# Performance work log

Hardware: AMD Instinct MI355X
Metric: run time of the kernel (lower is better)

Reference implementation:

```python
import jax, jax.numpy as jnp
import numpy as np

LOCAL_RADIUS = 127          # block_len = 128
TOKENS_PER_BLOCK = 16       # global_seq_len = L // 16
NEG = -1e9


def _concat_3_blocks(x):
    # x: [B, nb, bl, H, d] -> [B, nb, 3*bl, H, d] (prev, cur, next block; zero-padded ends)
    p = jnp.pad(x, [(0, 0), (1, 1), (0, 0), (0, 0), (0, 0)])
    return jnp.concatenate([p[:, :-2], p[:, 1:-1], p[:, 2:]], axis=2)


def _softmax_with_extra_logit(x, axis=-1):
    m = jnp.maximum(jax.lax.stop_gradient(x.max(axis, keepdims=True)), 0)
    unnorm = jnp.exp(x - m)
    denom = unnorm.sum(axis, keepdims=True) + jnp.exp(-m)
    return unnorm / denom


def setup_inputs() -> dict:
    key = jax.random.key(0)
    ks = jax.random.split(key, 5)
    B, L, D, H, dh = 2, 4096, 1024, 16, 64
    return {
        "x": jax.random.normal(ks[0], (B, L, D), jnp.float32),
        "Wq": jax.random.normal(ks[1], (D, H, dh), jnp.float32) * 0.02,
        "Wk": jax.random.normal(ks[2], (D, H, dh), jnp.float32) * 0.02,
        "Wv": jax.random.normal(ks[3], (D, H, dh), jnp.float32) * 0.02,
        "Wo": jax.random.normal(ks[4], (H, dh, D), jnp.float32) * 0.02,
    }


def reference(x, Wq, Wk, Wv, Wo):
    B, L, D = x.shape
    H, dh = Wq.shape[1], Wq.shape[2]
    bl = LOCAL_RADIUS + 1                      # block_len = 128
    nb = L // bl                               # num_blocks
    G = L // TOKENS_PER_BLOCK                  # global (side) seq len

    q = jnp.einsum("bld,dhk->blhk", x, Wq) / jnp.sqrt(jnp.asarray(dh, x.dtype))
    k = jnp.einsum("bld,dhk->blhk", x, Wk)
    v = jnp.einsum("bld,dhk->blhk", x, Wv)

    # transient-global aggregates: sum token embeddings within each block of TOKENS_PER_BLOCK
    block_ids = jnp.arange(L) // TOKENS_PER_BLOCK          # [L]
    one_hot = jax.nn.one_hot(block_ids, G, dtype=x.dtype)  # [L, G]
    g = jnp.einsum("bld,lg->bgd", x, one_hot)              # [B, G, D]
    side_k = jnp.einsum("bgd,dhk->bghk", g, Wk)
    side_v = jnp.einsum("bgd,dhk->bghk", g, Wv)

    # split into blocks and build 3-block sliding window keys/values
    qb = q.reshape(B, nb, bl, H, dh)
    kb = _concat_3_blocks(k.reshape(B, nb, bl, H, dh))     # [B, nb, 3bl, H, dh]
    vb = _concat_3_blocks(v.reshape(B, nb, bl, H, dh))

    k_cat = jnp.concatenate(
        [kb, jnp.broadcast_to(side_k[:, None], (B, nb, G, H, dh))], axis=2)
    v_cat = jnp.concatenate(
        [vb, jnp.broadcast_to(side_v[:, None], (B, nb, G, H, dh))], axis=2)

    # logits: [B, nb, H, bl, 3bl+G]
    logits = jnp.einsum("bnqhd,bnkhd->bnhqk", qb, k_cat)

    # local mask: enforce |rel| <= local_radius and in-bounds key positions
    q_idx = jnp.arange(bl)[:, None]                        # [bl, 1]
    k_idx = jnp.arange(3 * bl)[None, :]                    # [1, 3bl]
    rel = k_idx - bl - q_idx                               # relative position
    b_idx = jnp.arange(nb)[:, None, None]                  # [nb, 1, 1]
    k_pos = (b_idx - 1) * bl + k_idx                       # absolute key position
    valid = (jnp.abs(rel) <= LOCAL_RADIUS) & (k_pos >= 0) & (k_pos < L)
    local_bias = jnp.where(valid, 0.0, NEG).astype(logits.dtype)  # [nb, bl, 3bl]
    side_bias = jnp.zeros((nb, bl, G), logits.dtype)
    bias = jnp.concatenate([local_bias, side_bias], axis=-1)      # [nb, bl, 3bl+G]
    logits = logits + bias[None, :, None]

    probs = _softmax_with_extra_logit(logits, axis=-1)
    y = jnp.einsum("bnhqk,bnkhd->bnqhd", probs, v_cat)
    y = y.reshape(B, L, H, dh)
    return jnp.einsum("blhk,hkd->bld", y, Wo)
```

## Files before the change

kernel.cpp:

```cpp
#include <hip/hip_runtime.h>
#include <hip/hip_bf16.h>
#include <stdint.h>

#define SC_LOG2E 0.18033688011112042f

typedef __attribute__((ext_vector_type(8))) short short8;
typedef __attribute__((ext_vector_type(4))) short short4v;
typedef __attribute__((ext_vector_type(4))) float f32x4;

__device__ __forceinline__ unsigned short f2bf(float f) {
  unsigned int u = __float_as_uint(f);
  u += 0x7fffu + ((u >> 16) & 1u);
  return (unsigned short)(u >> 16);
}

__device__ __forceinline__ unsigned int pkbf(float a, float b) {
  union { __hip_bfloat162 h; unsigned int u; } cv;
  cv.h = __float22bfloat162_rn(float2{a, b});
  return cv.u;
}

__device__ __forceinline__ void gload_lds16(const void* g, void* l) {
  __builtin_amdgcn_global_load_lds((const __attribute__((address_space(1))) void*)g,
                                   (__attribute__((address_space(3))) void*)l,
                                   16, 0, 0);
}

__device__ __forceinline__ f32x4 mfma16(short8 a, short8 b, f32x4 c) {
  return __builtin_amdgcn_mfma_f32_16x16x32_bf16(a, b, c, 0, 0, 0);
}

__device__ __forceinline__ short4v tr_read(const unsigned short* p) {
  short4v r;
  asm volatile("ds_read_b64_tr_b16 %0, %1"
               : "=v"(r)
               : "v"((const __attribute__((address_space(3))) unsigned short*)p));
  return r;
}

__device__ __forceinline__ short8 cat44(short4v lo, short4v hi) {
  return __builtin_shufflevector(lo, hi, 0, 1, 2, 3, 4, 5, 6, 7);
}

__global__ __launch_bounds__(256) void prep_k(
    const float* __restrict__ x, unsigned short* __restrict__ xb,
    const float* __restrict__ wq, const float* __restrict__ wk,
    const float* __restrict__ wv, const float* __restrict__ wo,
    unsigned short* __restrict__ wqkv_t, unsigned short* __restrict__ wo_t) {
  __shared__ float tile[64 * 65];
  int bid = blockIdx.x;
  if (bid < 512) {
    int gr = bid;
    int c4 = threadIdx.x;
    const float4* p = (const float4*)(x + (size_t)gr * 16384) + c4;
#pragma unroll
    for (int t = 0; t < 16; ++t) {
      float4 v = p[(size_t)t * 256];
      ushort4 o;
      o.x = f2bf(v.x); o.y = f2bf(v.y); o.z = f2bf(v.z); o.w = f2bf(v.w);
      ((ushort4*)xb)[(size_t)(gr * 16 + t) * 256 + c4] = o;
    }
  } else {
    int idx = bid - 512;
    int z = idx >> 8, rem = idx & 255;
    const float* src = (z == 0) ? wq : (z == 1) ? wk : (z == 2) ? wv : wo;
    unsigned short* dst = (z == 3) ? wo_t : (wqkv_t + (size_t)z * 1048576);
    float scale = (z == 0) ? SC_LOG2E : 1.0f;
    int tc = (rem & 15) * 64, tr = (rem >> 4) * 64;
    int cx = threadIdx.x & 63, ry = threadIdx.x >> 6;
#pragma unroll
    for (int i = 0; i < 16; ++i) {
      int r = ry + i * 4;
      tile[r * 65 + cx] = src[(size_t)(tr + r) * 1024 + tc + cx];
    }
    __syncthreads();
#pragma unroll
    for (int i = 0; i < 16; ++i) {
      int r = ry + i * 4;
      dst[(size_t)(tc + r) * 1024 + tr + cx] = f2bf(tile[cx * 65 + r] * scale);
    }
  }
}

template <bool F32OUT, bool SIDE>
__global__ __launch_bounds__(256) void gemm_bt_k(
    const unsigned short* __restrict__ A, const unsigned short* __restrict__ Bt,
    void* __restrict__ Cv, int M, int N, int K, int nbn,
    unsigned short* __restrict__ sidekv) {
  __shared__ unsigned short Alds[128 * 64];
  __shared__ unsigned short Blds[128 * 64];
  int bid = blockIdx.x;
  int bm = bid / nbn, bn = bid % nbn;
  int lane = threadIdx.x & 63, wid = threadIdx.x >> 6;
  int wr = wid >> 1, wc = wid & 1;
  int l15 = lane & 15, lg = lane >> 4;

  f32x4 zero4 = {0.f, 0.f, 0.f, 0.f};
  f32x4 acc[4][4];
#pragma unroll
  for (int i = 0; i < 4; ++i)
#pragma unroll
    for (int j = 0; j < 4; ++j) acc[i][j] = zero4;

  int srow[4], scol[4];
#pragma unroll
  for (int i = 0; i < 4; ++i) {
    int seg = wid * 4 + i;
    int r = seg * 8 + (lane >> 3);
    srow[i] = r;
    scol[i] = ((lane & 7) ^ (r & 7)) * 8;
  }
  size_t arow0 = (size_t)bm * 128, brow0 = (size_t)bn * 128;

  int ksteps = K >> 6;
  for (int ks = 0; ks < ksteps; ++ks) {
    int k0 = ks << 6;
#pragma unroll
    for (int i = 0; i < 4; ++i) {
      gload_lds16(A + (arow0 + srow[i]) * K + k0 + scol[i],
                  (char*)Alds + (wid * 4 + i) * 1024);
      gload_lds16(Bt + (brow0 + srow[i]) * K + k0 + scol[i],
                  (char*)Blds + (wid * 4 + i) * 1024);
    }
    __syncthreads();
#pragma unroll
    for (int kk = 0; kk < 2; ++kk) {
      short8 af[4], bfr[4];
#pragma unroll
      for (int mi = 0; mi < 4; ++mi) {
        int r = wr * 64 + mi * 16 + l15;
        af[mi] = *(const short8*)((const char*)Alds + r * 128 +
                                  ((kk * 64 + lg * 16) ^ ((r & 7) << 4)));
      }
#pragma unroll
      for (int ni = 0; ni < 4; ++ni) {
        int r = wc * 64 + ni * 16 + l15;
        bfr[ni] = *(const short8*)((const char*)Blds + r * 128 +
                                   ((kk * 64 + lg * 16) ^ ((r & 7) << 4)));
      }
#pragma unroll
      for (int mi = 0; mi < 4; ++mi)
#pragma unroll
        for (int ni = 0; ni < 4; ++ni)
          acc[mi][ni] = mfma16(af[mi], bfr[ni], acc[mi][ni]);
    }
    __syncthreads();
  }
  int rq = lg << 2;
#pragma unroll
  for (int mi = 0; mi < 4; ++mi) {
    size_t row = arow0 + wr * 64 + mi * 16 + rq;
#pragma unroll
    for (int ni = 0; ni < 4; ++ni) {
      size_t col = brow0 + wc * 64 + ni * 16 + l15;
#pragma unroll
      for (int r = 0; r < 4; ++r) {
        if (F32OUT)
          ((float*)Cv)[(row + r) * N + col] = acc[mi][ni][r];
        else
          ((unsigned short*)Cv)[(row + r) * N + col] = f2bf(acc[mi][ni][r]);
      }
    }
  }
  if (SIDE && bn >= 8) {
    int gg = bm * 8 + wr * 4;
    int colb = bn * 128 - 1024 + wc * 64;
#pragma unroll
    for (int mi = 0; mi < 4; ++mi) {
#pragma unroll
      for (int ni = 0; ni < 4; ++ni) {
        float s = (acc[mi][ni][0] + acc[mi][ni][1]) +
                  (acc[mi][ni][2] + acc[mi][ni][3]);
        s += __shfl_xor(s, 16);
        s += __shfl_xor(s, 32);
        if (lg == 0)
          sidekv[(size_t)(gg + mi) * 2048 + colb + ni * 16 + l15] = f2bf(s);
      }
    }
  }
}

__global__ __launch_bounds__(512) void attn_k(
    const unsigned short* __restrict__ qkv,
    const unsigned short* __restrict__ side,
    unsigned short* __restrict__ y) {
  const int L = 4096, G = 256;
  __shared__ unsigned short K0[4096], V0[4096];
  __shared__ unsigned short K1[4096], V1[4096];
  __shared__ unsigned short Pt[8][1024];

  int bid = blockIdx.x;
  int n = bid & 15, h = (bid >> 4) & 15, b = bid >> 8;
  int lane = threadIdx.x & 63, wid = threadIdx.x >> 6;
  int l15 = lane & 15, lg = lane >> 4, rq = lg << 2;

  short8 qf[2][2];
  {
    size_t rowb = (size_t)b * L + n * 256 + wid * 32;
#pragma unroll
    for (int qt = 0; qt < 2; ++qt)
#pragma unroll
      for (int kk = 0; kk < 2; ++kk)
        qf[qt][kk] = *(const short8*)(qkv + (rowb + qt * 16 + l15) * 3072 +
                                      h * 64 + kk * 32 + lg * 8);
  }

  f32x4 zero4 = {0.f, 0.f, 0.f, 0.f};
  f32x4 accO[2][4], accSum[2];
#pragma unroll
  for (int qt = 0; qt < 2; ++qt) {
    accSum[qt] = zero4;
#pragma unroll
    for (int dt = 0; dt < 4; ++dt) accO[qt][dt] = zero4;
  }

  short8 onesf;
  {
    short o = (l15 == 0) ? (short)0x3F80 : (short)0;
    onesf = (short8){o, o, o, o, o, o, o, o};
  }

  int clo = (n == 0) ? 2 : 0, chi = (n == 15) ? 6 : 8;
  int nloc = chi - clo, goff = 8 - nloc;
  int m = nloc + 4;
  unsigned short* pt = Pt[wid];

  auto stage = [&](int c, unsigned short* Kl, unsigned short* Vl) {
    bool isg = c >= 8;
    int r = wid * 8 + (lane >> 3);
    int sl = ((lane & 7) ^ (r & 7)) * 8;
    int S = r;
    int di = S >> 4, ks = (S >> 3) & 1, lgg = (S >> 1) & 3, half = S & 1;
    int k = ks * 32 + lgg * 8 + half * 4 + ((lane & 7) >> 1);
    int d = di * 16 + (lane & 1) * 8;
    const unsigned short *ksrc, *vsrc;
    if (!isg) {
      int rowbase = b * L + n * 256 - 128 + c * 64;
      ksrc = qkv + (size_t)(rowbase + r) * 3072 + 1024 + h * 64 + sl;
      vsrc = qkv + (size_t)(rowbase + k) * 3072 + 2048 + h * 64 + d;
    } else {
      int rowbase = b * G + (c - 8) * 64;
      ksrc = side + (size_t)(rowbase + r) * 2048 + h * 64 + sl;
      vsrc = side + (size_t)(rowbase + k) * 2048 + 1024 + h * 64 + d;
    }
    gload_lds16(ksrc, (char*)Kl + wid * 1024);
    gload_lds16(vsrc, (char*)Vl + wid * 1024);
  };

  auto compute = [&](int c, const unsigned short* Kl, const unsigned short* Vl) {
    bool isg = c >= 8;
    int d0 = c * 64 - 128 - wid * 32;
    if (!isg) {
      if (d0 >= 159 || d0 <= -191) return;
    }
    bool partial = !isg && !(d0 >= -96 && d0 <= 64);

    f32x4 sacc[2][4];
#pragma unroll
    for (int qt = 0; qt < 2; ++qt)
#pragma unroll
      for (int kt = 0; kt < 4; ++kt) sacc[qt][kt] = zero4;
    __builtin_amdgcn_s_setprio(1);
#pragma unroll
    for (int kk = 0; kk < 2; ++kk) {
      short8 kf[4];
#pragma unroll
      for (int kt = 0; kt < 4; ++kt) {
        int r = kt * 16 + l15;
        kf[kt] = *(const short8*)((const char*)Kl + r * 128 +
                                  ((kk * 64 + lg * 16) ^ ((r & 7) << 4)));
      }
#pragma unroll
      for (int qt = 0; qt < 2; ++qt)
#pragma unroll
        for (int kt = 0; kt < 4; ++kt)
          sacc[qt][kt] = mfma16(qf[qt][kk], kf[kt], sacc[qt][kt]);
    }
    __builtin_amdgcn_s_setprio(0);
    if (partial) {
      int relc = d0 + l15 - rq;
#pragma unroll
      for (int qt = 0; qt < 2; ++qt)
#pragma unroll
        for (int kt = 0; kt < 4; ++kt)
#pragma unroll
          for (int r = 0; r < 4; ++r) {
            int rel = relc + kt * 16 - qt * 16 - r;
            sacc[qt][kt][r] =
                ((unsigned)(rel + 127) <= 254u) ? sacc[qt][kt][r] : -1e30f;
          }
    }
#pragma unroll
    for (int ks = 0; ks < 2; ++ks) {
#pragma unroll
      for (int qt = 0; qt < 2; ++qt)
#pragma unroll
        for (int k2 = 0; k2 < 2; ++k2) {
          int kt = ks * 2 + k2;
          uint2 pk;
          pk.x = pkbf(__builtin_amdgcn_exp2f(sacc[qt][kt][0]),
                      __builtin_amdgcn_exp2f(sacc[qt][kt][1]));
          pk.y = pkbf(__builtin_amdgcn_exp2f(sacc[qt][kt][2]),
                      __builtin_amdgcn_exp2f(sacc[qt][kt][3]));
          *(uint2*)(pt + (k2 * 8 + ((l15 >> 2) << 1) + qt) * 64 +
                    (l15 & 3) * 16 + rq) = pk;
        }
      asm volatile("s_waitcnt lgkmcnt(0)" ::: "memory");
      short4v palo[2], pahi[2], vlo[4], vhi[4];
#pragma unroll
      for (int qt = 0; qt < 2; ++qt) {
        const unsigned short* pb = pt + (lg * 4 + qt) * 64 + l15 * 4;
        palo[qt] = tr_read(pb);
        pahi[qt] = tr_read(pb + 128);
      }
#pragma unroll
      for (int dt = 0; dt < 4; ++dt) {
        const unsigned short* base =
            Vl + (((dt * 2 + ks) * 4 + lg) * 2) * 64 + l15 * 4;
        vlo[dt] = tr_read(base);
        vhi[dt] = tr_read(base + 64);
      }
      asm volatile("s_waitcnt lgkmcnt(0)" ::: "memory");
      __builtin_amdgcn_sched_barrier(0);
      __builtin_amdgcn_s_setprio(1);
#pragma unroll
      for (int qt = 0; qt < 2; ++qt) {
        short8 pa = cat44(palo[qt], pahi[qt]);
#pragma unroll
        for (int dt = 0; dt < 4; ++dt)
          accO[qt][dt] = mfma16(pa, cat44(vlo[dt], vhi[dt]), accO[qt][dt]);
        accSum[qt] = mfma16(pa, onesf, accSum[qt]);
      }
      __builtin_amdgcn_s_setprio(0);
    }
  };

  auto chunk_of = [&](int i) { return i < nloc ? i + clo : i + goff; };

  stage(chunk_of(0), K0, V0);
  __syncthreads();
  for (int i = 0; i < m; i += 2) {
    if (i + 1 < m) stage(chunk_of(i + 1), K1, V1);
    compute(chunk_of(i), K0, V0);
    __syncthreads();
    if (i + 1 >= m) break;
    if (i + 2 < m) stage(chunk_of(i + 2), K0, V0);
    compute(chunk_of(i + 1), K1, V1);
    __syncthreads();
  }

  size_t rowb = (size_t)b * L + n * 256 + wid * 32;
#pragma unroll
  for (int qt = 0; qt < 2; ++qt) {
    float inv[4];
#pragma unroll
    for (int r = 0; r < 4; ++r) {
      float s = __shfl(accSum[qt][r], lane & 48);
      inv[r] = 1.f / (1.f + s);
    }
#pragma unroll
    for (int dt = 0; dt < 4; ++dt) {
      int col = h * 64 + dt * 16 + l15;
#pragma unroll
      for (int r = 0; r < 4; ++r)
        y[(rowb + qt * 16 + rq + r) * 1024 + col] =
            f2bf(accO[qt][dt][r] * inv[r]);
    }
  }
}

extern "C" void kernel_launch(void* const* d_in, const int* in_sizes, int n_in,
                              void* d_out, int out_size, void* d_ws, size_t ws_size,
                              hipStream_t stream) {
  const float* x  = (const float*)d_in[0];
  const float* wq = (const float*)d_in[1];
  const float* wk = (const float*)d_in[2];
  const float* wv = (const float*)d_in[3];
  const float* wo = (const float*)d_in[4];
  char* ws = (char*)d_ws;
  const size_t MB = 1 << 20;
  unsigned short* xb     = (unsigned short*)(ws);
  unsigned short* wqkv_t = (unsigned short*)(ws + 17 * MB);
  unsigned short* wo_t   = (unsigned short*)(ws + 23 * MB);
  unsigned short* qkvb   = (unsigned short*)(ws + 25 * MB);
  unsigned short* sidekv = (unsigned short*)(ws + 73 * MB);
  unsigned short* yb     = xb;

  prep_k<<<1536, 256, 0, stream>>>(x, xb, wq, wk, wv, wo, wqkv_t, wo_t);
  gemm_bt_k<false, true><<<64 * 24, 256, 0, stream>>>(
      xb, wqkv_t, qkvb, 8192, 3072, 1024, 24, sidekv);
  attn_k<<<512, 512, 0, stream>>>(qkvb, sidekv, yb);
  gemm_bt_k<true, false><<<64 * 8, 256, 0, stream>>>(
      yb, wo_t, d_out, 8192, 1024, 1024, 8, nullptr);
}
```

Measured before the change: 151.1 us.

## Replace QKV projection GEMM with 256x256 tiled, double-buffered ping-pong kernel

Adds a new 512-thread GEMM for the QKV projection. It uses 256x256 output tiles, double-buffered LDS filled through direct global-to-LDS loads, and interleaves partial loads with MFMA phases under explicit waitcnt, barriers and s_setprio. It also remaps block IDs across eight XCD groups and keeps the fused side-KV reduction in the epilogue. The aim is more data reuse per tile and better overlap of memory and compute, at the cost of only 384 workgroups, which may underfill the CUs, and heavy register pressure.

```diff
diff --git a/kernel.cpp b/kernel.cpp
--- a/kernel.cpp
+++ b/kernel.cpp
@@ -82,11 +82,179 @@
   }
 }
 
-template <bool F32OUT, bool SIDE>
+__global__ __launch_bounds__(512, 2) void gemm256_k(
+    const unsigned short* __restrict__ A, const unsigned short* __restrict__ Bt,
+    unsigned short* __restrict__ C, int N, int K, int nbn,
+    unsigned short* __restrict__ sidekv) {
+  __shared__ unsigned short lds[2][2][16384];
+  int nwg = gridDim.x, cpx = nwg >> 3;
+  int bid = blockIdx.x;
+  bid = (bid & 7) * cpx + (bid >> 3);
+  int bm = bid / nbn, bn = bid % nbn;
+  int lane = threadIdx.x & 63, w = threadIdx.x >> 6;
+  int wm = w >> 2, wn = w & 3;
+  int l15 = lane & 15, lg = lane >> 4;
+  int lrow = lane >> 3;
+  int lcol = ((lane & 7) ^ lrow) * 8;
+  const int KT = K >> 6;
+
+  const unsigned short* Ab = A + ((size_t)bm * 256 + lrow) * K + lcol;
+  const unsigned short* Bb = Bt + ((size_t)bn * 256 + lrow) * K + lcol;
+
+  f32x4 zero4 = {0.f, 0.f, 0.f, 0.f};
+  f32x4 acc[8][4];
+#pragma unroll
+  for (int i = 0; i < 8; ++i)
+#pragma unroll
+    for (int j = 0; j < 4; ++j) acc[i][j] = zero4;
+
+  auto stage = [&](int kind, int t) {
+    if (t >= KT) return;
+    const unsigned short* src = (kind < 2) ? Ab : Bb;
+#pragma unroll
+    for (int i = 0; i < 2; ++i) {
+      int q = i * 64 + w * 8;
+      int r0;
+      if (kind == 0)      r0 = (q & 63) + ((q >> 6) << 7);
+      else if (kind == 1) r0 = (q & 63) + ((q >> 6) << 7) + 64;
+      else if (kind == 2) r0 = (q & 31) + ((q >> 5) << 6);
+      else                r0 = (q & 31) + ((q >> 5) << 6) + 32;
+      gload_lds16(src + (size_t)r0 * K + t * 64,
+                  &lds[t & 1][kind < 2 ? 0 : 1][r0 * 64]);
+    }
+  };
+  auto ldA = [&](const char* buf, int mi, int kk) -> short8 {
+    int r = wm * 128 + mi * 16 + l15;
+    return *(const short8*)(buf + r * 128 +
+                            2 * ((kk * 32 + lg * 8) ^ ((l15 & 7) * 8)));
+  };
+  auto ldB = [&](const char* buf, int ni, int kk) -> short8 {
+    int r = wn * 64 + ni * 16 + l15;
+    return *(const short8*)(buf + r * 128 +
+                            2 * ((kk * 32 + lg * 8) ^ ((l15 & 7) * 8)));
+  };
+
+  stage(0, 0); stage(2, 0); stage(3, 0); stage(1, 0);
+  asm volatile("s_waitcnt vmcnt(4)" ::: "memory");
+  __builtin_amdgcn_s_barrier();
+  __builtin_amdgcn_sched_barrier(0);
+
+  for (int t = 0; t < KT; ++t) {
+    const char* bufA = (const char*)&lds[t & 1][0][0];
+    const char* bufB = (const char*)&lds[t & 1][1][0];
+    bool nt = (t + 1 < KT);
+    short8 aF[4][2], b0[2][2], b1[2][2];
+#pragma unroll
+    for (int mi = 0; mi < 4; ++mi)
+#pragma unroll
+      for (int kk = 0; kk < 2; ++kk) aF[mi][kk] = ldA(bufA, mi, kk);
+#pragma unroll
+    for (int ni = 0; ni < 2; ++ni)
+#pragma unroll
+      for (int kk = 0; kk < 2; ++kk) b0[ni][kk] = ldB(bufB, ni, kk);
+    stage(0, t + 1);
+    if (nt) asm volatile("s_waitcnt vmcnt(4)" ::: "memory");
+    else    asm volatile("s_waitcnt vmcnt(2)" ::: "memory");
+    __builtin_amdgcn_s_barrier();
+    __builtin_amdgcn_sched_barrier(0);
+    __builtin_amdgcn_s_setprio(1);
+#pragma unroll
+    for (int kk = 0; kk < 2; ++kk)
+#pragma unroll
+      for (int mi = 0; mi < 4; ++mi)
+#pragma unroll
+        for (int ni = 0; ni < 2; ++ni)
+          acc[mi][ni] = mfma16(aF[mi][kk], b0[ni][kk], acc[mi][ni]);
+    __builtin_amdgcn_s_setprio(0);
+    __builtin_amdgcn_s_barrier();
+    __builtin_amdgcn_sched_barrier(0);
+#pragma unroll
+    for (int ni = 0; ni < 2; ++ni)
+#pragma unroll
+      for (int kk = 0; kk < 2; ++kk) b1[ni][kk] = ldB(bufB, ni + 2, kk);
+    stage(2, t + 1);
+    if (nt) asm volatile("s_waitcnt vmcnt(4)" ::: "memory");
+    else    asm volatile("s_waitcnt vmcnt(0)" ::: "memory");
+    __builtin_amdgcn_s_barrier();
+    __builtin_amdgcn_sched_barrier(0);
+    __builtin_amdgcn_s_setprio(1);
+#pragma unroll
+    for (int kk = 0; kk < 2; ++kk)
+#pragma unroll
+      for (int mi = 0; mi < 4; ++mi)
+#pragma unroll
+        for (int ni = 0; ni < 2; ++ni)
+          acc[mi][ni + 2] = mfma16(aF[mi][kk], b1[ni][kk], acc[mi][ni + 2]);
+    __builtin_amdgcn_s_setprio(0);
+    __builtin_amdgcn_s_barrier();
+    __builtin_amdgcn_sched_barrier(0);
+#pragma unroll
+    for (int mi = 0; mi < 4; ++mi)
+#pragma unroll
+      for (int kk = 0; kk < 2; ++kk) aF[mi][kk] = ldA(bufA, mi + 4, kk);
+    stage(3, t + 1);
+    __builtin_amdgcn_s_barrier();
+    __builtin_amdgcn_sched_barrier(0);
+    __builtin_amdgcn_s_setprio(1);
+#pragma unroll
+    for (int kk = 0; kk < 2; ++kk)
+#pragma unroll
+      for (int mi = 0; mi < 4; ++mi)
+#pragma unroll
+        for (int ni = 0; ni < 2; ++ni)
+          acc[mi + 4][ni + 2] = mfma16(aF[mi][kk], b1[ni][kk], acc[mi + 4][ni + 2]);
+    __builtin_amdgcn_s_setprio(0);
+    __builtin_amdgcn_s_barrier();
+    __builtin_amdgcn_sched_barrier(0);
+    stage(1, t + 1);
+    if (nt) asm volatile("s_waitcnt vmcnt(4)" ::: "memory");
+    __builtin_amdgcn_s_barrier();
+    __builtin_amdgcn_sched_barrier(0);
+    __builtin_amdgcn_s_setprio(1);
+#pragma unroll
+    for (int kk = 0; kk < 2; ++kk)
+#pragma unroll
+      for (int mi = 0; mi < 4; ++mi)
+#pragma unroll
+        for (int ni = 0; ni < 2; ++ni)
+          acc[mi + 4][ni] = mfma16(aF[mi][kk], b0[ni][kk], acc[mi + 4][ni]);
+    __builtin_amdgcn_s_setprio(0);
+    __builtin_amdgcn_s_barrier();
+    __builtin_amdgcn_sched_barrier(0);
+  }
+
+#pragma unroll
+  for (int mi = 0; mi < 8; ++mi) {
+    size_t row = (size_t)bm * 256 + wm * 128 + mi * 16 + lg * 4;
+#pragma unroll
+    for (int ni = 0; ni < 4; ++ni) {
+      size_t col = (size_t)bn * 256 + wn * 64 + ni * 16 + l15;
+#pragma unroll
+      for (int r = 0; r < 4; ++r)
+        C[(row + r) * N + col] = f2bf(acc[mi][ni][r]);
+    }
+  }
+  if (sidekv && bn >= 4) {
+    int gg = bm * 16 + wm * 8;
+    int colb = bn * 256 - 1024 + wn * 64;
+#pragma unroll
+    for (int mi = 0; mi < 8; ++mi) {
+#pragma unroll
+      for (int ni = 0; ni < 4; ++ni) {
+        float s = (acc[mi][ni][0] + acc[mi][ni][1]) +
+                  (acc[mi][ni][2] + acc[mi][ni][3]);
+        s += __shfl_xor(s, 16);
+        s += __shfl_xor(s, 32);
+        if (lg == 0)
+          sidekv[(size_t)(gg + mi) * 2048 + colb + ni * 16 + l15] = f2bf(s);
+      }
+    }
+  }
+}
+
 __global__ __launch_bounds__(256) void gemm_bt_k(
     const unsigned short* __restrict__ A, const unsigned short* __restrict__ Bt,
-    void* __restrict__ Cv, int M, int N, int K, int nbn,
-    unsigned short* __restrict__ sidekv) {
+    float* __restrict__ Cv, int N, int K, int nbn) {
   __shared__ unsigned short Alds[128 * 64];
   __shared__ unsigned short Blds[128 * 64];
   int bid = blockIdx.x;
@@ -154,28 +322,8 @@
     for (int ni = 0; ni < 4; ++ni) {
       size_t col = brow0 + wc * 64 + ni * 16 + l15;
 #pragma unroll
-      for (int r = 0; r < 4; ++r) {
-        if (F32OUT)
-          ((float*)Cv)[(row + r) * N + col] = acc[mi][ni][r];
-        else
-          ((unsigned short*)Cv)[(row + r) * N + col] = f2bf(acc[mi][ni][r]);
-      }
-    }
-  }
-  if (SIDE && bn >= 8) {
-    int gg = bm * 8 + wr * 4;
-    int colb = bn * 128 - 1024 + wc * 64;
-#pragma unroll
-    for (int mi = 0; mi < 4; ++mi) {
-#pragma unroll
-      for (int ni = 0; ni < 4; ++ni) {
-        float s = (acc[mi][ni][0] + acc[mi][ni][1]) +
-                  (acc[mi][ni][2] + acc[mi][ni][3]);
-        s += __shfl_xor(s, 16);
-        s += __shfl_xor(s, 32);
-        if (lg == 0)
-          sidekv[(size_t)(gg + mi) * 2048 + colb + ni * 16 + l15] = f2bf(s);
-      }
+      for (int r = 0; r < 4; ++r)
+        Cv[(row + r) * N + col] = acc[mi][ni][r];
     }
   }
 }
@@ -387,9 +535,7 @@
   unsigned short* yb     = xb;
 
   prep_k<<<1536, 256, 0, stream>>>(x, xb, wq, wk, wv, wo, wqkv_t, wo_t);
-  gemm_bt_k<false, true><<<64 * 24, 256, 0, stream>>>(
-      xb, wqkv_t, qkvb, 8192, 3072, 1024, 24, sidekv);
+  gemm256_k<<<32 * 12, 512, 0, stream>>>(xb, wqkv_t, qkvb, 3072, 1024, 12, sidekv);
   attn_k<<<512, 512, 0, stream>>>(qkvb, sidekv, yb);
-  gemm_bt_k<true, false><<<64 * 8, 256, 0, stream>>>(
-      yb, wo_t, d_out, 8192, 1024, 1024, 8, nullptr);
-}
+  gemm_bt_k<<<64 * 8, 256, 0, stream>>>(yb, wo_t, (float*)d_out, 1024, 1024, 8);
+}
```

New measurement: 153.7 us. Within noise of the previous version (+1.7%).
